# Optimization experiments

Hardware: AMD Instinct MI355X
Metric: run time of the kernel (lower is better)

## Reference

```python
import jax, jax.numpy as jnp
import numpy as np

N, E = 100000, 1600000
NODE_IN, EDGE_IN, H = 128, 16, 128


def sage_conv(x, src, dst, Wl, Wr, b, n_nodes):
    # PyG SAGEConv (aggr='mean'): out = lin_l(mean_{j->i} x_j) + lin_r(x_i), bias on lin_l
    msg_sum = jax.ops.segment_sum(x[src], dst, num_segments=n_nodes)      # [N, d]
    cnt = jax.ops.segment_sum(jnp.ones((src.shape[0],), x.dtype), dst, num_segments=n_nodes)
    mean = msg_sum / jnp.maximum(cnt, 1.0)[:, None]                        # empty neighborhoods -> 0
    return mean @ Wl + x @ Wr + b


def setup_inputs() -> dict:
    key = jax.random.key(0)
    ks = jax.random.split(key, 12)
    s = lambda d: 1.0 / np.sqrt(d)
    return {
        "x": jax.random.normal(ks[0], (N, NODE_IN), jnp.float32),
        "edge_index": jax.random.randint(ks[1], (2, E), 0, N, dtype=jnp.int64),
        "edge_attr": jax.random.normal(ks[2], (E, EDGE_IN), jnp.float32),
        "Wl1": jax.random.normal(ks[3], (NODE_IN, H), jnp.float32) * s(NODE_IN),
        "Wr1": jax.random.normal(ks[4], (NODE_IN, H), jnp.float32) * s(NODE_IN),
        "b1": jnp.zeros((H,), jnp.float32),
        "Wl2": jax.random.normal(ks[5], (H, H), jnp.float32) * s(H),
        "Wr2": jax.random.normal(ks[6], (H, H), jnp.float32) * s(H),
        "b2": jnp.zeros((H,), jnp.float32),
        "Wm1": jax.random.normal(ks[7], (2 * H + EDGE_IN, H), jnp.float32) * s(2 * H + EDGE_IN),
        "bm1": jnp.zeros((H,), jnp.float32),
        "Wm2": jax.random.normal(ks[8], (H, 1), jnp.float32) * s(H),
        "bm2": jnp.zeros((1,), jnp.float32),
    }


def reference(x, edge_index, edge_attr, Wl1, Wr1, b1, Wl2, Wr2, b2, Wm1, bm1, Wm2, bm2):
    src, dst = edge_index[0], edge_index[1]
    h = jax.nn.relu(sage_conv(x, src, dst, Wl1, Wr1, b1, N))
    h = jax.nn.relu(sage_conv(h, src, dst, Wl2, Wr2, b2, N))
    edge_feat = jnp.concatenate([h[src], h[dst], edge_attr], axis=1)  # [E, 2H+edge_in]
    out = jax.nn.relu(edge_feat @ Wm1 + bm1) @ Wm2 + bm2               # dropout is identity in eval
    return out.reshape(-1)
```

## Files before the change

### kernel.cpp

```cpp
#include <hip/hip_runtime.h>

typedef _Float16 f16;
typedef _Float16 f16x8 __attribute__((ext_vector_type(8)));
typedef float f32x4 __attribute__((ext_vector_type(4)));

#define MFMA16(a,b,c) __builtin_amdgcn_mfma_f32_16x16x32_f16((a),(b),(c),0,0,0)

__global__ void k_detect(const long long* ei, int n_nodes, int* flag) {
    long long v = ei[threadIdx.x];
    int bad = (v < 0 || v >= n_nodes);
    unsigned long long m = __ballot(bad);
    if (threadIdx.x == 0) *flag = (m == 0ULL);
}

__global__ void k_idx(const void* ei, int E, const int* __restrict__ flag,
                      int* __restrict__ src, int* __restrict__ dst) {
    int e = blockIdx.x * 256 + threadIdx.x;
    if (e >= E) return;
    if (*flag) {
        const long long* p = (const long long*)ei;
        src[e] = (int)p[e];
        dst[e] = (int)p[(size_t)E + e];
    } else {
        const int* p = (const int*)ei;
        src[e] = p[e];
        dst[e] = p[(size_t)E + e];
    }
}

__global__ void k_x2h(const float* __restrict__ x, f16* __restrict__ xh, int n) {
    int i = (blockIdx.x * 256 + threadIdx.x) * 8;
    if (i >= n) return;
    float4 a = *(const float4*)(x + i);
    float4 b = *(const float4*)(x + i + 4);
    f16x8 h;
    h[0] = (f16)a.x; h[1] = (f16)a.y; h[2] = (f16)a.z; h[3] = (f16)a.w;
    h[4] = (f16)b.x; h[5] = (f16)b.y; h[6] = (f16)b.z; h[7] = (f16)b.w;
    *(f16x8*)(xh + i) = h;
}

__global__ void k_wfrag(const float* __restrict__ Wa, const float* __restrict__ Wb,
                        f16* __restrict__ dst, int KS) {
    int t = blockIdx.x * 256 + threadIdx.x;
    int total = KS * 8 * 64;
    if (t >= total) return;
    int l = t & 63;
    int s = t >> 9;
    int k0 = s * 32 + (l >> 4) * 8;
    int j = ((t >> 6) & 7) * 16 + (l & 15);
    f16x8 h;
    #pragma unroll
    for (int e = 0; e < 8; e++) {
        int k = k0 + e;
        float v = (k < 128) ? Wa[k * 128 + j] : Wb[(k - 128) * 128 + j];
        h[e] = (f16)v;
    }
    *(f16x8*)(dst + (size_t)t * 8) = h;
}

__global__ void k_zfrag(const float* __restrict__ Wm1, f16* __restrict__ dst) {
    int t = blockIdx.x * 256 + threadIdx.x;
    if (t >= 4 * 16 * 64) return;
    int lane = t & 63, c = (t >> 6) & 15, s = t >> 10;
    int k0 = s * 32 + (lane >> 4) * 8;
    int j = c * 16 + (lane & 15);
    f16x8 h;
    #pragma unroll
    for (int e = 0; e < 8; e++) {
        int k = k0 + e;
        float v = (j < 128) ? Wm1[k * 128 + j] : Wm1[(128 + k) * 128 + (j - 128)];
        h[e] = (f16)v;
    }
    *(f16x8*)(dst + (size_t)t * 8) = h;
}

__global__ void k_wefrag(const float* __restrict__ Wm1, f16* __restrict__ dst) {
    int t = blockIdx.x * 256 + threadIdx.x;
    if (t >= 8 * 64) return;
    int lane = t & 63, ct = t >> 6;
    int k0 = (lane >> 4) * 8;
    int j = ct * 16 + (lane & 15);
    f16x8 h;
    #pragma unroll
    for (int e = 0; e < 8; e++) {
        int k = k0 + e;
        h[e] = (k < 16) ? (f16)Wm1[(256 + k) * 128 + j] : (f16)0.0f;
    }
    *(f16x8*)(dst + (size_t)t * 8) = h;
}

__global__ void k_hist(const int* __restrict__ dst, int E, int* __restrict__ deg) {
    int e = blockIdx.x * 256 + threadIdx.x;
    if (e < E) atomicAdd(&deg[dst[e]], 1);
}

__global__ void k_bsum(const int* __restrict__ deg, int n, int* __restrict__ bsum) {
    __shared__ int ws[4];
    const int tid = threadIdx.x;
    int i = blockIdx.x * 1024 + tid * 4;
    int s = 0;
    if (i + 3 < n) {
        int4 d = *(const int4*)(deg + i);
        s = d.x + d.y + d.z + d.w;
    } else {
        #pragma unroll
        for (int j = 0; j < 4; j++) if (i + j < n) s += deg[i + j];
    }
    #pragma unroll
    for (int m = 1; m < 64; m <<= 1) s += __shfl_xor(s, m, 64);
    if ((tid & 63) == 0) ws[tid >> 6] = s;
    __syncthreads();
    if (tid == 0) bsum[blockIdx.x] = ws[0] + ws[1] + ws[2] + ws[3];
}

__global__ void k_bscan(int* __restrict__ bsum, int nb, int* __restrict__ rowptr_n) {
    __shared__ int wsum[4];
    const int tid = threadIdx.x, lane = tid & 63, wid = tid >> 6;
    int v = (tid < nb) ? bsum[tid] : 0;
    int inc = v;
    #pragma unroll
    for (int off = 1; off < 64; off <<= 1) {
        int u = __shfl_up(inc, off, 64);
        if (lane >= off) inc += u;
    }
    if (lane == 63) wsum[wid] = inc;
    __syncthreads();
    int woff = 0;
    for (int j = 0; j < wid; j++) woff += wsum[j];
    int excl = woff + inc - v;
    if (tid < nb) bsum[tid] = excl;
    if (tid == nb - 1) rowptr_n[0] = excl + v;
}

__global__ void k_rowptr(const int* __restrict__ deg, int n, const int* __restrict__ boff,
                         int* __restrict__ rowptr, int* __restrict__ cursor) {
    __shared__ int wsum[4];
    const int tid = threadIdx.x, lane = tid & 63, wid = tid >> 6;
    int i = blockIdx.x * 1024 + tid * 4;
    int d0 = 0, d1 = 0, d2 = 0, d3 = 0;
    if (i + 3 < n) {
        int4 d = *(const int4*)(deg + i);
        d0 = d.x; d1 = d.y; d2 = d.z; d3 = d.w;
    } else {
        if (i     < n) d0 = deg[i];
        if (i + 1 < n) d1 = deg[i + 1];
        if (i + 2 < n) d2 = deg[i + 2];
        if (i + 3 < n) d3 = deg[i + 3];
    }
    int s = d0 + d1 + d2 + d3;
    int inc = s;
    #pragma unroll
    for (int off = 1; off < 64; off <<= 1) {
        int u = __shfl_up(inc, off, 64);
        if (lane >= off) inc += u;
    }
    if (lane == 63) wsum[wid] = inc;
    __syncthreads();
    int woff = 0;
    for (int j = 0; j < wid; j++) woff += wsum[j];
    int excl = boff[blockIdx.x] + woff + inc - s;
    int e1 = excl + d0, e2 = e1 + d1, e3 = e2 + d2;
    if (i     < n) { rowptr[i]     = excl; cursor[i]     = excl; }
    if (i + 1 < n) { rowptr[i + 1] = e1;   cursor[i + 1] = e1; }
    if (i + 2 < n) { rowptr[i + 2] = e2;   cursor[i + 2] = e2; }
    if (i + 3 < n) { rowptr[i + 3] = e3;   cursor[i + 3] = e3; }
}

__global__ void k_scatter(const int* __restrict__ src, const int* __restrict__ dst, int E,
                          int* __restrict__ cursor, int* __restrict__ col) {
    int e = blockIdx.x * 256 + threadIdx.x;
    if (e < E) {
        int p = atomicAdd(&cursor[dst[e]], 1);
        col[p] = src[e];
    }
}

__global__ __launch_bounds__(256) void k_agg(
    const f16* __restrict__ tab, const int* __restrict__ rowptr,
    const int* __restrict__ col, f16* __restrict__ mean, int n_nodes) {
    const int tid = threadIdx.x;
    const int node = blockIdx.x * 16 + (tid >> 4);
    const int c = tid & 15;
    if (node >= n_nodes) return;
    const int s0 = rowptr[node], s1 = rowptr[node + 1];
    float acc[8] = {0.f, 0.f, 0.f, 0.f, 0.f, 0.f, 0.f, 0.f};
    int k = s0;
    for (; k + 3 < s1; k += 4) {
        const int n0 = col[k], n1 = col[k + 1], n2 = col[k + 2], n3 = col[k + 3];
        f16x8 v0 = *(const f16x8*)(tab + (size_t)n0 * 128 + c * 8);
        f16x8 v1 = *(const f16x8*)(tab + (size_t)n1 * 128 + c * 8);
        f16x8 v2 = *(const f16x8*)(tab + (size_t)n2 * 128 + c * 8);
        f16x8 v3 = *(const f16x8*)(tab + (size_t)n3 * 128 + c * 8);
        #pragma unroll
        for (int j = 0; j < 8; j++)
            acc[j] += ((float)v0[j] + (float)v1[j]) + ((float)v2[j] + (float)v3[j]);
    }
    for (; k < s1; ++k) {
        const int n0 = col[k];
        f16x8 v0 = *(const f16x8*)(tab + (size_t)n0 * 128 + c * 8);
        #pragma unroll
        for (int j = 0; j < 8; j++) acc[j] += (float)v0[j];
    }
    int d = s1 - s0; if (d < 1) d = 1;
    const float inv = 1.f / (float)d;
    f16x8 r;
    #pragma unroll
    for (int j = 0; j < 8; j++) r[j] = (f16)(acc[j] * inv);
    *(f16x8*)(mean + (size_t)node * 128 + c * 8) = r;
}

__global__ __launch_bounds__(256, 2) void k_gemm_sage(
    const f16* __restrict__ A1, const f16* __restrict__ A2,
    const f16* __restrict__ Wf, const float* __restrict__ bias,
    f16* __restrict__ out, int n_rows, int iters, int gridW) {
    __shared__ __align__(16) f16 sW[8 * 8 * 64 * 8];
    const int tid = threadIdx.x, lane = tid & 63, w = tid >> 6;
    const int l15 = lane & 15, g = lane >> 4;
    for (int i = tid; i < 8 * 8 * 64; i += 256)
        *(uint4*)&sW[(size_t)i * 8] = *(const uint4*)&Wf[(size_t)i * 8];
    __syncthreads();
    const int c0 = (2 * w) * 16 + l15, c1 = (2 * w + 1) * 16 + l15;
    const float b0 = bias[c0], b1 = bias[c1];
    for (int it = 0; it < iters; ++it) {
        const int base = (blockIdx.x + it * gridW) * 64;
        if (base >= n_rows) break;
        f32x4 acc[4][2];
        #pragma unroll
        for (int t = 0; t < 4; t++) {
            acc[t][0] = f32x4{b0, b0, b0, b0};
            acc[t][1] = f32x4{b1, b1, b1, b1};
        }
        #pragma unroll
        for (int s = 0; s < 8; s++) {
            const f16* Asrc = (s < 4) ? A1 : A2;
            const int koff = (s & 3) * 32 + g * 8;
            f16x8 bf0 = *(const f16x8*)&sW[((s * 8 + 2 * w    ) * 64 + lane) * 8];
            f16x8 bf1 = *(const f16x8*)&sW[((s * 8 + 2 * w + 1) * 64 + lane) * 8];
            #pragma unroll
            for (int t = 0; t < 4; t++) {
                int row = base + t * 16 + l15;
                if (row >= n_rows) row = n_rows - 1;
                f16x8 a = *(const f16x8*)(Asrc + (size_t)row * 128 + koff);
                acc[t][0] = MFMA16(a, bf0, acc[t][0]);
                acc[t][1] = MFMA16(a, bf1, acc[t][1]);
            }
        }
        #pragma unroll
        for (int t = 0; t < 4; t++) {
            #pragma unroll
            for (int i = 0; i < 4; i++) {
                int row = base + t * 16 + g * 4 + i;
                if (row < n_rows) {
                    float v0 = acc[t][0][i]; v0 = v0 > 0.f ? v0 : 0.f;
                    float v1 = acc[t][1][i]; v1 = v1 > 0.f ? v1 : 0.f;
                    out[(size_t)row * 128 + c0] = (f16)v0;
                    out[(size_t)row * 128 + c1] = (f16)v1;
                }
            }
        }
    }
}

__global__ __launch_bounds__(256, 2) void k_zgemm(
    const f16* __restrict__ h2, const f16* __restrict__ zwf,
    const float* __restrict__ bm1, f16* __restrict__ z,
    int n_rows, int iters, int gridW) {
    const int tid = threadIdx.x, lane = tid & 63, w = tid >> 6;
    const int l15 = lane & 15, g = lane >> 4;
    f16x8 wf[4][4];
    #pragma unroll
    for (int s = 0; s < 4; s++)
        #pragma unroll
        for (int cc = 0; cc < 4; cc++)
            wf[s][cc] = *(const f16x8*)(zwf + ((size_t)((s * 16 + 4 * w + cc) * 64 + lane)) * 8);
    float bias[4];
    #pragma unroll
    for (int cc = 0; cc < 4; cc++) {
        int j = (4 * w + cc) * 16 + l15;
        bias[cc] = (j >= 128) ? bm1[j - 128] : 0.0f;
    }
    for (int it = 0; it < iters; ++it) {
        const int base = (blockIdx.x + it * gridW) * 64;
        if (base >= n_rows) break;
        f32x4 acc[4][4];
        #pragma unroll
        for (int t = 0; t < 4; t++)
            #pragma unroll
            for (int cc = 0; cc < 4; cc++)
                acc[t][cc] = f32x4{bias[cc], bias[cc], bias[cc], bias[cc]};
        #pragma unroll
        for (int s = 0; s < 4; s++) {
            f16x8 a[4];
            #pragma unroll
            for (int t = 0; t < 4; t++) {
                int row = base + t * 16 + l15;
                if (row >= n_rows) row = n_rows - 1;
                a[t] = *(const f16x8*)(h2 + (size_t)row * 128 + s * 32 + g * 8);
            }
            #pragma unroll
            for (int cc = 0; cc < 4; cc++)
                #pragma unroll
                for (int t = 0; t < 4; t++)
                    acc[t][cc] = MFMA16(a[t], wf[s][cc], acc[t][cc]);
        }
        #pragma unroll
        for (int t = 0; t < 4; t++)
            #pragma unroll
            for (int cc = 0; cc < 4; cc++)
                #pragma unroll
                for (int i = 0; i < 4; i++) {
                    int row = base + t * 16 + g * 4 + i;
                    if (row < n_rows)
                        z[(size_t)row * 256 + (4 * w + cc) * 16 + l15] = (f16)acc[t][cc][i];
                }
    }
}

#define ZP 136
__global__ __launch_bounds__(256, 4) void k_edge2(
    const f16* __restrict__ z, const float* __restrict__ ea,
    const int* __restrict__ src, const int* __restrict__ dst,
    const f16* __restrict__ wef, const float* __restrict__ Wm2,
    const float* __restrict__ bm2, float* __restrict__ out,
    int E, int iters, int gridW) {
    __shared__ __align__(16) f16 sZ[64 * ZP];
    __shared__ __align__(16) f16 sEA[4 * 64 * 8];
    __shared__ float sPart[4][64];
    const int tid = threadIdx.x, lane = tid & 63, w = tid >> 6;
    const int l15 = lane & 15, g = lane >> 4;
    const int sr = lane >> 2, sq = lane & 3;
    const int slot_s = w * 16 + sr;

    for (int i = tid; i < 4 * 64; i += 256)
        *(f16x8*)(&sEA[0] + (size_t)i * 8) = f16x8{};

    const f16x8 be0 = *(const f16x8*)(wef + ((size_t)((2 * w) * 64 + lane)) * 8);
    const f16x8 be1 = *(const f16x8*)(wef + ((size_t)((2 * w + 1) * 64 + lane)) * 8);
    const float w20 = Wm2[(2 * w) * 16 + l15];
    const float w21 = Wm2[(2 * w + 1) * 16 + l15];
    const float bv = bm2[0];

    f16x8 zs[4], zd[4];
    union { f16 h[4]; uint2 u2; } eh;

    auto stage_load = [&](int ebase) {
        int er = ebase + slot_s; if (er > E - 1) er = E - 1;
        const int is = src[er], id = dst[er];
        const f16* ps = z + (size_t)is * 256 + sq * 32;
        const f16* pd = z + (size_t)id * 256 + 128 + sq * 32;
        #pragma unroll
        for (int i = 0; i < 4; i++) {
            zs[i] = *(const f16x8*)(ps + i * 8);
            zd[i] = *(const f16x8*)(pd + i * 8);
        }
        float4 ev = *(const float4*)(ea + (size_t)er * 16 + sq * 4);
        eh.h[0] = (f16)ev.x; eh.h[1] = (f16)ev.y; eh.h[2] = (f16)ev.z; eh.h[3] = (f16)ev.w;
    };
    auto stage_write = [&]() {
        f16* zp = &sZ[0] + slot_s * ZP + sq * 32;
        #pragma unroll
        for (int i = 0; i < 4; i++) {
            f16x8 v = zs[i] + zd[i];
            *(f16x8*)(zp + i * 8) = v;
        }
        f16* ep = &sEA[0] +
                  ((size_t)((slot_s >> 4) * 64 + (sq >> 1) * 16 + (slot_s & 15)) * 8 + (sq & 1) * 4);
        *(uint2*)ep = eh.u2;
    };

    stage_load(blockIdx.x * 64);
    __syncthreads();
    stage_write();
    __syncthreads();

    for (int it = 0; it < iters; ++it) {
        const int ebase = (blockIdx.x + it * gridW) * 64;
        if (ebase >= E) break;
        const int nxt = (blockIdx.x + (it + 1) * gridW) * 64;
        const bool has_next = (it + 1 < iters) && (nxt < E);
        if (has_next) stage_load(nxt);

        f32x4 acc[4][2];
        #pragma unroll
        for (int t = 0; t < 4; t++) { acc[t][0] = f32x4{0,0,0,0}; acc[t][1] = f32x4{0,0,0,0}; }
        #pragma unroll
        for (int t = 0; t < 4; t++) {
            f16x8 a = *(const f16x8*)(&sEA[0] + ((size_t)(t * 64 + lane)) * 8);
            acc[t][0] = MFMA16(a, be0, acc[t][0]);
            acc[t][1] = MFMA16(a, be1, acc[t][1]);
        }
        #pragma unroll
        for (int t = 0; t < 4; t++) {
            float p[4];
            #pragma unroll
            for (int i = 0; i < 4; i++) {
                int slot = t * 16 + g * 4 + i;
                float z0 = (float)sZ[slot * ZP + (2 * w) * 16 + l15];
                float z1 = (float)sZ[slot * ZP + (2 * w + 1) * 16 + l15];
                float v0 = z0 + acc[t][0][i]; v0 = v0 > 0.f ? v0 : 0.f;
                float v1 = z1 + acc[t][1][i]; v1 = v1 > 0.f ? v1 : 0.f;
                p[i] = v0 * w20 + v1 * w21;
            }
            #pragma unroll
            for (int m = 1; m < 16; m <<= 1)
                #pragma unroll
                for (int i = 0; i < 4; i++) p[i] += __shfl_xor(p[i], m, 64);
            if (l15 == 0)
                #pragma unroll
                for (int i = 0; i < 4; i++) sPart[w][t * 16 + g * 4 + i] = p[i];
        }
        __syncthreads();
        if (tid < 64) {
            int e = ebase + tid;
            if (e < E)
                out[e] = sPart[0][tid] + sPart[1][tid] + sPart[2][tid] + sPart[3][tid] + bv;
        }
        if (has_next) stage_write();
        __syncthreads();
    }
}

extern "C" void kernel_launch(void* const* d_in, const int* in_sizes, int n_in,
                              void* d_out, int out_size, void* d_ws, size_t ws_size,
                              hipStream_t stream) {
    const float* x   = (const float*)d_in[0];
    const void*  ei  = d_in[1];
    const float* ea  = (const float*)d_in[2];
    const float* Wl1 = (const float*)d_in[3];
    const float* Wr1 = (const float*)d_in[4];
    const float* b1  = (const float*)d_in[5];
    const float* Wl2 = (const float*)d_in[6];
    const float* Wr2 = (const float*)d_in[7];
    const float* b2  = (const float*)d_in[8];
    const float* Wm1 = (const float*)d_in[9];
    const float* bm1 = (const float*)d_in[10];
    const float* Wm2 = (const float*)d_in[11];
    const float* bm2 = (const float*)d_in[12];

    const int N = in_sizes[0] / 128;
    const int E = in_sizes[1] / 2;

    char* ws = (char*)d_ws;
    size_t off = 0;
    auto alloc = [&](size_t bytes) -> void* {
        void* p = ws + off;
        off = (off + bytes + 255) & ~(size_t)255;
        return p;
    };
    f16* xh     = (f16*)alloc((size_t)N * 128 * 2);
    f16* mean   = (f16*)alloc((size_t)N * 128 * 2);
    f16* h1     = (f16*)alloc((size_t)N * 128 * 2);
    int* src    = (int*)alloc((size_t)E * 4);
    int* dst    = (int*)alloc((size_t)E * 4);
    int* col    = (int*)alloc((size_t)E * 4);
    int* deg    = (int*)alloc((size_t)N * 4);
    int* rowptr = (int*)alloc((size_t)(N + 1) * 4);
    int* cursor = (int*)alloc((size_t)N * 4);
    int* bsum   = (int*)alloc((size_t)1024 * 4);
    f16* w1f    = (f16*)alloc((size_t)8 * 8 * 64 * 8 * 2);
    f16* w2f    = (f16*)alloc((size_t)8 * 8 * 64 * 8 * 2);
    f16* zwf    = (f16*)alloc((size_t)4 * 16 * 64 * 8 * 2);
    f16* wef    = (f16*)alloc((size_t)8 * 64 * 8 * 2);
    int* flag   = (int*)alloc(4);
    if (off > ws_size) return;
    f16* h2 = xh;
    f16* z  = mean;

    const int eb = (E + 255) / 256;
    const int nbk = (N + 1023) / 1024;

    k_detect<<<1, 64, 0, stream>>>((const long long*)ei, N, flag);
    k_idx<<<eb, 256, 0, stream>>>(ei, E, flag, src, dst);
    k_x2h<<<(N * 128 / 8 + 255) / 256, 256, 0, stream>>>(x, xh, N * 128);
    k_wfrag<<<16, 256, 0, stream>>>(Wl1, Wr1, w1f, 8);
    k_wfrag<<<16, 256, 0, stream>>>(Wl2, Wr2, w2f, 8);
    k_zfrag<<<16, 256, 0, stream>>>(Wm1, zwf);
    k_wefrag<<<2, 256, 0, stream>>>(Wm1, wef);

    hipMemsetAsync(deg, 0, (size_t)N * 4, stream);
    k_hist<<<eb, 256, 0, stream>>>(dst, E, deg);
    k_bsum<<<nbk, 256, 0, stream>>>(deg, N, bsum);
    k_bscan<<<1, 256, 0, stream>>>(bsum, nbk, rowptr + N);
    k_rowptr<<<nbk, 256, 0, stream>>>(deg, N, bsum, rowptr, cursor);
    k_scatter<<<eb, 256, 0, stream>>>(src, dst, E, cursor, col);

    const int gridW = 512;
    const int rb = (N + 63) / 64;
    const int g_iters = (rb + gridW - 1) / gridW;
    const int ag = (N + 15) / 16;

    k_agg<<<ag, 256, 0, stream>>>(xh, rowptr, col, mean, N);
    k_gemm_sage<<<gridW, 256, 0, stream>>>(mean, xh, w1f, b1, h1, N, g_iters, gridW);
    k_agg<<<ag, 256, 0, stream>>>(h1, rowptr, col, mean, N);
    k_gemm_sage<<<gridW, 256, 0, stream>>>(mean, h1, w2f, b2, h2, N, g_iters, gridW);

    const int zg = 512;
    const int z_iters = (rb + zg - 1) / zg;
    k_zgemm<<<zg, 256, 0, stream>>>(h2, zwf, bm1, z, N, z_iters, zg);

    const int eg = 1792;
    const int nb = (E + 63) / 64;
    const int e_iters = (nb + eg - 1) / eg;
    k_edge2<<<eg, 256, 0, stream>>>(z, ea, src, dst, wef, Wm2, bm2,
                                    (float*)d_out, E, e_iters, eg);
}
```

Baseline: 591.4 us.

## Fuse neighbor aggregation, SAGE GEMM and edge-projection GEMM into per-tile kernels

Replaces the separate aggregation, SAGE GEMM and z-projection kernels with one templated kernel per layer. The kernel aggregates 64 node means into LDS, multiplies them by the weights, and in the second layer writes the ReLU'd h2 back to LDS and computes the z projection directly. This removes the round trips of the mean and h2 tensors through global memory and cuts kernel launches. In exchange, weight fragments are now read from global memory per block instead of staged in LDS, and the grid is one tile per block rather than persistent. The z buffer now aliases xh, which is safe only because layer 2 no longer reads xh.

```diff
diff --git a/kernel.cpp b/kernel.cpp
--- a/kernel.cpp
+++ b/kernel.cpp
@@ -175,76 +175,83 @@
     }
 }
 
-__global__ __launch_bounds__(256) void k_agg(
-    const f16* __restrict__ tab, const int* __restrict__ rowptr,
-    const int* __restrict__ col, f16* __restrict__ mean, int n_nodes) {
-    const int tid = threadIdx.x;
-    const int node = blockIdx.x * 16 + (tid >> 4);
-    const int c = tid & 15;
-    if (node >= n_nodes) return;
-    const int s0 = rowptr[node], s1 = rowptr[node + 1];
-    float acc[8] = {0.f, 0.f, 0.f, 0.f, 0.f, 0.f, 0.f, 0.f};
-    int k = s0;
-    for (; k + 3 < s1; k += 4) {
-        const int n0 = col[k], n1 = col[k + 1], n2 = col[k + 2], n3 = col[k + 3];
-        f16x8 v0 = *(const f16x8*)(tab + (size_t)n0 * 128 + c * 8);
-        f16x8 v1 = *(const f16x8*)(tab + (size_t)n1 * 128 + c * 8);
-        f16x8 v2 = *(const f16x8*)(tab + (size_t)n2 * 128 + c * 8);
-        f16x8 v3 = *(const f16x8*)(tab + (size_t)n3 * 128 + c * 8);
-        #pragma unroll
-        for (int j = 0; j < 8; j++)
-            acc[j] += ((float)v0[j] + (float)v1[j]) + ((float)v2[j] + (float)v3[j]);
-    }
-    for (; k < s1; ++k) {
-        const int n0 = col[k];
-        f16x8 v0 = *(const f16x8*)(tab + (size_t)n0 * 128 + c * 8);
-        #pragma unroll
-        for (int j = 0; j < 8; j++) acc[j] += (float)v0[j];
-    }
-    int d = s1 - s0; if (d < 1) d = 1;
-    const float inv = 1.f / (float)d;
-    f16x8 r;
-    #pragma unroll
-    for (int j = 0; j < 8; j++) r[j] = (f16)(acc[j] * inv);
-    *(f16x8*)(mean + (size_t)node * 128 + c * 8) = r;
-}
-
-__global__ __launch_bounds__(256, 2) void k_gemm_sage(
-    const f16* __restrict__ A1, const f16* __restrict__ A2,
+#define AP 136
+template<int DO_Z>
+__global__ __launch_bounds__(256, DO_Z ? 3 : 4) void k_fuse(
+    const f16* __restrict__ tab,
+    const int* __restrict__ rowptr, const int* __restrict__ col,
     const f16* __restrict__ Wf, const float* __restrict__ bias,
-    f16* __restrict__ out, int n_rows, int iters, int gridW) {
-    __shared__ __align__(16) f16 sW[8 * 8 * 64 * 8];
+    const f16* __restrict__ zwf, const float* __restrict__ bm1,
+    f16* __restrict__ out, int n_rows) {
+    __shared__ __align__(16) f16 sA[64 * AP];
     const int tid = threadIdx.x, lane = tid & 63, w = tid >> 6;
     const int l15 = lane & 15, g = lane >> 4;
-    for (int i = tid; i < 8 * 8 * 64; i += 256)
-        *(uint4*)&sW[(size_t)i * 8] = *(const uint4*)&Wf[(size_t)i * 8];
-    __syncthreads();
-    const int c0 = (2 * w) * 16 + l15, c1 = (2 * w + 1) * 16 + l15;
+    const int base = blockIdx.x * 64;
+
+    const int g16 = tid >> 4, c = tid & 15;
+    #pragma unroll
+    for (int rep = 0; rep < 4; rep++) {
+        const int node = base + rep * 16 + g16;
+        float acc[8] = {0.f, 0.f, 0.f, 0.f, 0.f, 0.f, 0.f, 0.f};
+        int d = 1;
+        if (node < n_rows) {
+            const int s0 = rowptr[node], s1 = rowptr[node + 1];
+            int k = s0;
+            for (; k + 3 < s1; k += 4) {
+                const int n0 = col[k], n1 = col[k + 1], n2 = col[k + 2], n3 = col[k + 3];
+                f16x8 v0 = *(const f16x8*)(tab + (size_t)n0 * 128 + c * 8);
+                f16x8 v1 = *(const f16x8*)(tab + (size_t)n1 * 128 + c * 8);
+                f16x8 v2 = *(const f16x8*)(tab + (size_t)n2 * 128 + c * 8);
+                f16x8 v3 = *(const f16x8*)(tab + (size_t)n3 * 128 + c * 8);
+                #pragma unroll
+                for (int j = 0; j < 8; j++)
+                    acc[j] += ((float)v0[j] + (float)v1[j]) + ((float)v2[j] + (float)v3[j]);
+            }
+            for (; k < s1; ++k) {
+                const int n0 = col[k];
+                f16x8 v0 = *(const f16x8*)(tab + (size_t)n0 * 128 + c * 8);
+                #pragma unroll
+                for (int j = 0; j < 8; j++) acc[j] += (float)v0[j];
+            }
+            d = s1 - s0; if (d < 1) d = 1;
+        }
+        const float inv = 1.f / (float)d;
+        f16x8 r;
+        #pragma unroll
+        for (int j = 0; j < 8; j++) r[j] = (f16)(acc[j] * inv);
+        *(f16x8*)&sA[(rep * 16 + g16) * AP + c * 8] = r;
+    }
+    __syncthreads();
+
+    const int c0 = (2 * w) * 16 + l15, c1 = c0 + 16;
     const float b0 = bias[c0], b1 = bias[c1];
-    for (int it = 0; it < iters; ++it) {
-        const int base = (blockIdx.x + it * gridW) * 64;
-        if (base >= n_rows) break;
-        f32x4 acc[4][2];
+    f32x4 acc[4][2];
+    #pragma unroll
+    for (int t = 0; t < 4; t++) {
+        acc[t][0] = f32x4{b0, b0, b0, b0};
+        acc[t][1] = f32x4{b1, b1, b1, b1};
+    }
+    #pragma unroll
+    for (int s = 0; s < 8; s++) {
+        f16x8 bf0 = *(const f16x8*)&Wf[((size_t)(s * 8 + 2 * w    ) * 64 + lane) * 8];
+        f16x8 bf1 = *(const f16x8*)&Wf[((size_t)(s * 8 + 2 * w + 1) * 64 + lane) * 8];
+        const int koff = (s & 3) * 32 + g * 8;
         #pragma unroll
         for (int t = 0; t < 4; t++) {
-            acc[t][0] = f32x4{b0, b0, b0, b0};
-            acc[t][1] = f32x4{b1, b1, b1, b1};
-        }
-        #pragma unroll
-        for (int s = 0; s < 8; s++) {
-            const f16* Asrc = (s < 4) ? A1 : A2;
-            const int koff = (s & 3) * 32 + g * 8;
-            f16x8 bf0 = *(const f16x8*)&sW[((s * 8 + 2 * w    ) * 64 + lane) * 8];
-            f16x8 bf1 = *(const f16x8*)&sW[((s * 8 + 2 * w + 1) * 64 + lane) * 8];
-            #pragma unroll
-            for (int t = 0; t < 4; t++) {
+            f16x8 a;
+            if (s < 4) {
+                a = *(const f16x8*)&sA[(t * 16 + l15) * AP + koff];
+            } else {
                 int row = base + t * 16 + l15;
                 if (row >= n_rows) row = n_rows - 1;
-                f16x8 a = *(const f16x8*)(Asrc + (size_t)row * 128 + koff);
-                acc[t][0] = MFMA16(a, bf0, acc[t][0]);
-                acc[t][1] = MFMA16(a, bf1, acc[t][1]);
-            }
-        }
+                a = *(const f16x8*)(tab + (size_t)row * 128 + koff);
+            }
+            acc[t][0] = MFMA16(a, bf0, acc[t][0]);
+            acc[t][1] = MFMA16(a, bf1, acc[t][1]);
+        }
+    }
+
+    if (DO_Z == 0) {
         #pragma unroll
         for (int t = 0; t < 4; t++) {
             #pragma unroll
@@ -258,61 +265,55 @@
                 }
             }
         }
-    }
-}
-
-__global__ __launch_bounds__(256, 2) void k_zgemm(
-    const f16* __restrict__ h2, const f16* __restrict__ zwf,
-    const float* __restrict__ bm1, f16* __restrict__ z,
-    int n_rows, int iters, int gridW) {
-    const int tid = threadIdx.x, lane = tid & 63, w = tid >> 6;
-    const int l15 = lane & 15, g = lane >> 4;
-    f16x8 wf[4][4];
-    #pragma unroll
-    for (int s = 0; s < 4; s++)
-        #pragma unroll
-        for (int cc = 0; cc < 4; cc++)
-            wf[s][cc] = *(const f16x8*)(zwf + ((size_t)((s * 16 + 4 * w + cc) * 64 + lane)) * 8);
-    float bias[4];
-    #pragma unroll
-    for (int cc = 0; cc < 4; cc++) {
-        int j = (4 * w + cc) * 16 + l15;
-        bias[cc] = (j >= 128) ? bm1[j - 128] : 0.0f;
-    }
-    for (int it = 0; it < iters; ++it) {
-        const int base = (blockIdx.x + it * gridW) * 64;
-        if (base >= n_rows) break;
-        f32x4 acc[4][4];
-        #pragma unroll
-        for (int t = 0; t < 4; t++)
-            #pragma unroll
-            for (int cc = 0; cc < 4; cc++)
-                acc[t][cc] = f32x4{bias[cc], bias[cc], bias[cc], bias[cc]};
-        #pragma unroll
-        for (int s = 0; s < 4; s++) {
-            f16x8 a[4];
+    } else {
+        __syncthreads();
+        #pragma unroll
+        for (int t = 0; t < 4; t++) {
+            #pragma unroll
+            for (int i = 0; i < 4; i++) {
+                const int rl = t * 16 + g * 4 + i;
+                float v0 = acc[t][0][i]; v0 = v0 > 0.f ? v0 : 0.f;
+                float v1 = acc[t][1][i]; v1 = v1 > 0.f ? v1 : 0.f;
+                sA[rl * AP + c0] = (f16)v0;
+                sA[rl * AP + c1] = (f16)v1;
+            }
+        }
+        __syncthreads();
+        #pragma unroll
+        for (int half = 0; half < 2; half++) {
+            const int j0 = (4 * w + 2 * half) * 16 + l15, j1 = j0 + 16;
+            const float zb0 = (j0 >= 128) ? bm1[j0 - 128] : 0.0f;
+            const float zb1 = (j1 >= 128) ? bm1[j1 - 128] : 0.0f;
+            f32x4 zacc[4][2];
             #pragma unroll
             for (int t = 0; t < 4; t++) {
-                int row = base + t * 16 + l15;
-                if (row >= n_rows) row = n_rows - 1;
-                a[t] = *(const f16x8*)(h2 + (size_t)row * 128 + s * 32 + g * 8);
-            }
-            #pragma unroll
-            for (int cc = 0; cc < 4; cc++)
-                #pragma unroll
-                for (int t = 0; t < 4; t++)
-                    acc[t][cc] = MFMA16(a[t], wf[s][cc], acc[t][cc]);
-        }
-        #pragma unroll
-        for (int t = 0; t < 4; t++)
-            #pragma unroll
-            for (int cc = 0; cc < 4; cc++)
+                zacc[t][0] = f32x4{zb0, zb0, zb0, zb0};
+                zacc[t][1] = f32x4{zb1, zb1, zb1, zb1};
+            }
+            #pragma unroll
+            for (int s = 0; s < 4; s++) {
+                f16x8 wf0 = *(const f16x8*)&zwf[((size_t)(s * 16 + 4 * w + 2 * half    ) * 64 + lane) * 8];
+                f16x8 wf1 = *(const f16x8*)&zwf[((size_t)(s * 16 + 4 * w + 2 * half + 1) * 64 + lane) * 8];
+                const int koff = s * 32 + g * 8;
+                #pragma unroll
+                for (int t = 0; t < 4; t++) {
+                    f16x8 a = *(const f16x8*)&sA[(t * 16 + l15) * AP + koff];
+                    zacc[t][0] = MFMA16(a, wf0, zacc[t][0]);
+                    zacc[t][1] = MFMA16(a, wf1, zacc[t][1]);
+                }
+            }
+            #pragma unroll
+            for (int t = 0; t < 4; t++) {
                 #pragma unroll
                 for (int i = 0; i < 4; i++) {
                     int row = base + t * 16 + g * 4 + i;
-                    if (row < n_rows)
-                        z[(size_t)row * 256 + (4 * w + cc) * 16 + l15] = (f16)acc[t][cc][i];
+                    if (row < n_rows) {
+                        out[(size_t)row * 256 + j0] = (f16)zacc[t][0][i];
+                        out[(size_t)row * 256 + j1] = (f16)zacc[t][1][i];
+                    }
                 }
+            }
+        }
     }
 }
 
@@ -447,8 +448,8 @@
         off = (off + bytes + 255) & ~(size_t)255;
         return p;
     };
-    f16* xh     = (f16*)alloc((size_t)N * 128 * 2);
-    f16* mean   = (f16*)alloc((size_t)N * 128 * 2);
+    f16* z      = (f16*)alloc((size_t)N * 256 * 2);
+    f16* xh     = z;
     f16* h1     = (f16*)alloc((size_t)N * 128 * 2);
     int* src    = (int*)alloc((size_t)E * 4);
     int* dst    = (int*)alloc((size_t)E * 4);
@@ -463,11 +464,10 @@
     f16* wef    = (f16*)alloc((size_t)8 * 64 * 8 * 2);
     int* flag   = (int*)alloc(4);
     if (off > ws_size) return;
-    f16* h2 = xh;
-    f16* z  = mean;
 
     const int eb = (E + 255) / 256;
     const int nbk = (N + 1023) / 1024;
+    const int rb64 = (N + 63) / 64;
 
     k_detect<<<1, 64, 0, stream>>>((const long long*)ei, N, flag);
     k_idx<<<eb, 256, 0, stream>>>(ei, E, flag, src, dst);
@@ -484,19 +484,8 @@
     k_rowptr<<<nbk, 256, 0, stream>>>(deg, N, bsum, rowptr, cursor);
     k_scatter<<<eb, 256, 0, stream>>>(src, dst, E, cursor, col);
 
-    const int gridW = 512;
-    const int rb = (N + 63) / 64;
-    const int g_iters = (rb + gridW - 1) / gridW;
-    const int ag = (N + 15) / 16;
-
-    k_agg<<<ag, 256, 0, stream>>>(xh, rowptr, col, mean, N);
-    k_gemm_sage<<<gridW, 256, 0, stream>>>(mean, xh, w1f, b1, h1, N, g_iters, gridW);
-    k_agg<<<ag, 256, 0, stream>>>(h1, rowptr, col, mean, N);
-    k_gemm_sage<<<gridW, 256, 0, stream>>>(mean, h1, w2f, b2, h2, N, g_iters, gridW);
-
-    const int zg = 512;
-    const int z_iters = (rb + zg - 1) / zg;
-    k_zgemm<<<zg, 256, 0, stream>>>(h2, zwf, bm1, z, N, z_iters, zg);
+    k_fuse<0><<<rb64, 256, 0, stream>>>(xh, rowptr, col, w1f, b1, nullptr, nullptr, h1, N);
+    k_fuse<1><<<rb64, 256, 0, stream>>>(h1, rowptr, col, w2f, b2, zwf, bm1, z, N);
 
     const int eg = 1792;
     const int nb = (E + 63) / 64;
```

Result: faster. 570.8 us (-3.5%).
